# Optimization experiments

Measured on AMD Instinct MI355X. Metric: run time of the kernel, lower is better.

The kernel has to match this reference:

```python
import jax, jax.numpy as jnp
import numpy as np

B, NB, NV, H = 512, 3, 64, 256
CS = (40, 40)          # child branch lengths
COUP = (16, 48)        # parent vertices where child branches attach
IN = 9


def setup_inputs() -> dict:
    key = jax.random.key(0)
    ks = jax.random.split(key, 24)

    def w(k, shape, fan_in):
        return jax.random.uniform(k, shape, jnp.float32, -1.0, 1.0) / np.sqrt(fan_in)

    return {
        "current_vertices": jax.random.normal(ks[0], (B, NB, NV, 3), jnp.float32),
        "previous_vertices": jax.random.normal(ks[1], (B, NB, NV, 3), jnp.float32),
        "clamped_target_hints": jax.random.normal(ks[2], (B, NB, NV, 3), jnp.float32),
        # encoder
        "enc_w1": w(ks[3], (IN, H), IN), "enc_b1": w(ks[4], (H,), IN),
        "enc_w2": w(ks[5], (H, H), H), "enc_b2": w(ks[6], (H,), H),
        # child-sum tree-LSTM cell (bottom-up)
        "W_iou": w(ks[7], (H, 3 * H), H), "b_iou": w(ks[8], (3 * H,), H),
        "U_iou": w(ks[9], (H, 3 * H), H),
        "W_f": w(ks[10], (H, H), H), "b_f": w(ks[11], (H,), H),
        "U_f": w(ks[12], (H, H), H),
        # torch.nn.LSTMCell (top-down), gate order i,f,g,o
        "W_ih": w(ks[13], (H, 4 * H), H), "b_ih": w(ks[14], (4 * H,), H),
        "W_hh": w(ks[15], (H, 4 * H), H), "b_hh": w(ks[16], (4 * H,), H),
        # decoder
        "dec_w1": w(ks[17], (2 * H, H), 2 * H), "dec_b1": w(ks[18], (H,), 2 * H),
        "dec_w2": w(ks[19], (H, 3), H), "dec_b2": w(ks[20], (3,), H),
    }


def _forward(cv, pv, hints,
             enc_w1, enc_b1, enc_w2, enc_b2,
             W_iou, b_iou, U_iou, W_f, b_f, U_f,
             W_ih, b_ih, W_hh, b_hh,
             dec_w1, dec_b1, dec_w2, dec_b2):
    Bsz = cv.shape[0]
    nv = cv.shape[2]
    dt = cv.dtype
    feats = jnp.concatenate([cv, cv - pv, hints], axis=-1)            # [B,NB,NV,9]
    enc = jnp.maximum(feats @ enc_w1 + enc_b1, 0.0) @ enc_w2 + enc_b2  # [B,NB,NV,H]
    zero = jnp.zeros((Bsz, H), dt)

    # --- bottom-up: child-sum cell. A leaf with a single all-zero child is
    # mathematically identical to a zero initial carry (U_* have no bias),
    # so each chain is a plain scan from leaf toward vertex 0.
    def bu_chain_step(carry, x):
        h_prev, c_prev = carry
        iou = x @ W_iou + b_iou + h_prev @ U_iou
        i, o, u = jnp.split(iou, 3, axis=-1)
        f = jax.nn.sigmoid(x @ W_f + b_f + h_prev @ U_f)
        c = jax.nn.sigmoid(i) * jnp.tanh(u) + f * c_prev
        h = jax.nn.sigmoid(o) * jnp.tanh(c)
        return (h, c), (h, c)

    # child branches: leaf (v=L-1) -> v=0
    roots_h, roots_c, child_bu = [], [], []
    for k, L in enumerate(CS):
        xs = jnp.transpose(enc[:, k + 1, :L], (1, 0, 2))[::-1]  # time-major, reversed
        _, (hs, cs) = jax.lax.scan(bu_chain_step, (zero, zero), xs)
        hs, cs = hs[::-1], cs[::-1]                              # [L,B,H] indexed by v
        roots_h.append(hs[0]); roots_c.append(cs[0])
        child_bu.append((hs, cs))

    # coupled-child states injected at coupling vertices of the parent chain
    K = len(CS)
    coup_h = jnp.zeros((nv, K, Bsz, H), dt)
    coup_c = jnp.zeros_like(coup_h)
    coup_m = jnp.zeros((nv, K), dt)
    for k, ci in enumerate(COUP):
        coup_h = coup_h.at[ci, k].set(roots_h[k])
        coup_c = coup_c.at[ci, k].set(roots_c[k])
        coup_m = coup_m.at[ci, k].set(1.0)

    def bu_parent_step(carry, inp):
        h_prev, c_prev = carry
        x, ch, cc, m = inp  # ch,cc: [K,B,H]; m: [K]
        h_sum = h_prev + (m[:, None, None] * ch).sum(0)
        iou = x @ W_iou + b_iou + h_sum @ U_iou
        i, o, u = jnp.split(iou, 3, axis=-1)
        wf = x @ W_f + b_f
        fc = jax.nn.sigmoid(wf + h_prev @ U_f) * c_prev
        fc = fc + (m[:, None, None] * jax.nn.sigmoid(wf[None] + ch @ U_f) * cc).sum(0)
        c = jax.nn.sigmoid(i) * jnp.tanh(u) + fc
        h = jax.nn.sigmoid(o) * jnp.tanh(c)
        return (h, c), (h, c)

    xs0 = jnp.transpose(enc[:, 0], (1, 0, 2))  # [NV,B,H]
    _, (p_hs, p_cs) = jax.lax.scan(
        bu_parent_step, (zero, zero),
        (xs0[::-1], coup_h[::-1], coup_c[::-1], coup_m[::-1]))
    p_hs, p_cs = p_hs[::-1], p_cs[::-1]

    bu_h = jnp.zeros((Bsz, NB, nv, H), dt)
    bu_c = jnp.zeros_like(bu_h)
    bu_h = bu_h.at[:, 0].set(jnp.transpose(p_hs, (1, 0, 2)))
    bu_c = bu_c.at[:, 0].set(jnp.transpose(p_cs, (1, 0, 2)))
    for k, L in enumerate(CS):
        hs, cs = child_bu[k]
        bu_h = bu_h.at[:, k + 1, :L].set(jnp.transpose(hs, (1, 0, 2)))
        bu_c = bu_c.at[:, k + 1, :L].set(jnp.transpose(cs, (1, 0, 2)))

    # --- top-down: standard LSTMCell chains
    def td_step(carry, x):
        h, c = carry
        g = x @ W_ih + b_ih + h @ W_hh + b_hh
        i, f, gg, o = jnp.split(g, 4, axis=-1)
        c = jax.nn.sigmoid(f) * c + jax.nn.sigmoid(i) * jnp.tanh(gg)
        h = jax.nn.sigmoid(o) * jnp.tanh(c)
        return (h, c), (h, c)

    _, (t_hs, t_cs) = jax.lax.scan(td_step, (bu_h[:, 0, 0], bu_c[:, 0, 0]), xs0[1:])
    td_p_h = jnp.concatenate([bu_h[:, 0, 0][None], t_hs], 0)  # [NV,B,H]
    td_p_c = jnp.concatenate([bu_c[:, 0, 0][None], t_cs], 0)

    td_h = jnp.zeros_like(bu_h)
    td_h = td_h.at[:, 0].set(jnp.transpose(td_p_h, (1, 0, 2)))
    for k, L in enumerate(CS):
        xs = jnp.transpose(enc[:, k + 1, :L], (1, 0, 2))
        _, (hs, _) = jax.lax.scan(td_step, (td_p_h[COUP[k]], td_p_c[COUP[k]]), xs)
        td_h = td_h.at[:, k + 1, :L].set(jnp.transpose(hs, (1, 0, 2)))

    comb = jnp.concatenate([bu_h, td_h], axis=-1)  # [B,NB,NV,2H]
    delta = jnp.maximum(comb @ dec_w1 + dec_b1, 0.0) @ dec_w2 + dec_b2
    pred = cv + delta
    mask = jnp.ones((NB, nv, 1), dt)
    for k, L in enumerate(CS):
        mask = mask.at[k + 1, L:].set(0.0)
    return pred * mask[None]


def reference(current_vertices, previous_vertices, clamped_target_hints,
              enc_w1, enc_b1, enc_w2, enc_b2,
              W_iou, b_iou, U_iou, W_f, b_f, U_f,
              W_ih, b_ih, W_hh, b_hh,
              dec_w1, dec_b1, dec_w2, dec_b2):
    return _forward(current_vertices, previous_vertices, clamped_target_hints,
                    enc_w1, enc_b1, enc_w2, enc_b2,
                    W_iou, b_iou, U_iou, W_f, b_f, U_f,
                    W_ih, b_ih, W_hh, b_hh,
                    dec_w1, dec_b1, dec_w2, dec_b2)
```

## Files before the change

kernel.cpp:

```cpp
#include <hip/hip_runtime.h>
#include <hip/hip_bf16.h>
#include <hip/hip_fp8.h>


constexpr int Hd    = 256;
constexpr int NBv   = 3;
constexpr int NVv   = 64;
constexpr int BATCH = 512;
constexpr long long NROWS = (long long)BATCH * NBv * NVv;
constexpr int CLEN = 40;
constexpr int CI0 = 16, CI1 = 48;

typedef __hip_bfloat16 bf16;
typedef unsigned short ushort;
typedef unsigned char u8;
typedef __attribute__((ext_vector_type(8))) short short8;
typedef __attribute__((ext_vector_type(4))) float f32x4;
typedef __attribute__((ext_vector_type(2))) long longx2;

__device__ __forceinline__ float sigf(float x)   { return 1.f / (1.f + __expf(-x)); }
__device__ __forceinline__ float tanh_f(float x) { return 1.f - 2.f / (__expf(2.f * x) + 1.f); }

__device__ __forceinline__ ushort f2bf(float x) {
  unsigned u = __float_as_uint(x);
  return (ushort)((u + 0x7FFFu + ((u >> 16) & 1u)) >> 16);
}
__device__ __forceinline__ float bf2f(ushort u) {
  return __uint_as_float(((unsigned)u) << 16);
}
__device__ __forceinline__ u8 f2fp8(float x) {
  __hip_fp8_e4m3 q(x);
  return (u8)q.__x;
}

#define STEPSYNC() { \
    asm volatile("s_waitcnt lgkmcnt(0)" ::: "memory"); \
    __builtin_amdgcn_s_barrier(); }

__global__ __launch_bounds__(256) void pack_bu8_kernel(
    const float* __restrict__ W_iou, const float* __restrict__ W_f,
    const float* __restrict__ U_iou, const float* __restrict__ U_f,
    u8* __restrict__ out)
{
  int u = blockIdx.x * 256 + threadIdx.x;
  int s = u & 1, l = (u >> 1) & 63, T = u >> 7;
  int kp = T & 7, nt = T >> 3;
  int ks = kp * 2 + s;
  int k0 = ks * 32 + (l >> 4) * 8;
  int n  = nt * 16 + (l & 15);
  unsigned long long r = 0;
#pragma unroll
  for (int j = 0; j < 8; ++j) {
    int k = k0 + j;
    float v;
    if (k < 256) v = (n < 768) ? W_iou[k * 768 + n] : W_f[k * 256 + (n - 768)];
    else         v = (n < 768) ? U_iou[(k - 256) * 768 + n] : U_f[(k - 256) * 256 + (n - 768)];
    r |= ((unsigned long long)f2fp8(v)) << (8 * j);
  }
  *(unsigned long long*)(out + (size_t)u * 8) = r;
}

__global__ __launch_bounds__(256) void pack_td8_kernel(
    const float* __restrict__ W_ih, const float* __restrict__ W_hh,
    u8* __restrict__ out)
{
  int u = blockIdx.x * 256 + threadIdx.x;
  int s = u & 1, l = (u >> 1) & 63, T = u >> 7;
  int kp = T & 7, nt = T >> 3;
  int ks = kp * 2 + s;
  int k0 = ks * 32 + (l >> 4) * 8;
  int n  = nt * 16 + (l & 15);
  unsigned long long r = 0;
#pragma unroll
  for (int j = 0; j < 8; ++j) {
    int k = k0 + j;
    float v = (k < 256) ? W_ih[k * 1024 + n] : W_hh[(k - 256) * 1024 + n];
    r |= ((unsigned long long)f2fp8(v)) << (8 * j);
  }
  *(unsigned long long*)(out + (size_t)u * 8) = r;
}

__global__ __launch_bounds__(256) void pack_wfx8_kernel(
    const float* __restrict__ W_f, u8* __restrict__ out)
{
  int u = blockIdx.x * 256 + threadIdx.x;
  int s = u & 1, l = (u >> 1) & 63, T = u >> 7;
  int kp = T & 3, nt = T >> 2;
  int ks = kp * 2 + s;
  int k0 = ks * 32 + (l >> 4) * 8;
  int n  = nt * 16 + (l & 15);
  unsigned long long r = 0;
#pragma unroll
  for (int j = 0; j < 8; ++j)
    r |= ((unsigned long long)f2fp8(W_f[(k0 + j) * 256 + n])) << (8 * j);
  *(unsigned long long*)(out + (size_t)u * 8) = r;
}

__global__ __launch_bounds__(256) void pack_encw2_kernel(
    const float* __restrict__ w2, ushort* __restrict__ out)
{
  int idx = blockIdx.x * 256 + threadIdx.x;
  int j = idx & 7, l = (idx >> 3) & 63, T = idx >> 9;
  int ks = T & 7, nt = T >> 3;
  int k = ks * 32 + (l >> 4) * 8 + j;
  int n = nt * 16 + (l & 15);
  out[idx] = f2bf(w2[k * 256 + n]);
}

__global__ __launch_bounds__(256) void pack_decw1_kernel(
    const float* __restrict__ w1, ushort* __restrict__ out)
{
  int idx = blockIdx.x * 256 + threadIdx.x;
  int j = idx & 7, l = (idx >> 3) & 63, T = idx >> 9;
  int ks = T & 15, nt = T >> 4;
  int k = ks * 32 + (l >> 4) * 8 + j;
  int n = nt * 16 + (l & 15);
  out[idx] = f2bf(w1[k * 256 + n]);
}

__global__ __launch_bounds__(256) void pack_decw2_kernel(
    const float* __restrict__ w2, ushort* __restrict__ out)
{
  int idx = blockIdx.x * 256 + threadIdx.x;
  int j = idx & 7, l = (idx >> 3) & 63, T = idx >> 9;
  int ks = T & 7;
  int k = ks * 32 + (l >> 4) * 8 + j;
  int n = l & 15;
  out[idx] = (n < 3) ? f2bf(w2[k * 3 + n]) : (ushort)0;
}

__device__ __forceinline__ short8 ldA16(const ushort* buf, int row, int kbyte) {
  int off = (row * 512 + kbyte) ^ ((row & 7) << 4);
  return *(const short8*)((const char*)buf + off);
}
__device__ __forceinline__ short8 ldA1024(const ushort* buf, int row, int kbyte) {
  int off = (row * 1024 + kbyte) ^ ((row & 7) << 4);
  return *(const short8*)((const char*)buf + off);
}
#define STA(BUF, R, JJ, BITS) { \
    int off_ = ((R) * 512 + (JJ) * 2) ^ (((R) & 7) << 4); \
    (BUF)[off_ >> 1] = (BITS); }
#define STA8(BUF, R, JJ, B8) { \
    int off_ = ((R) * 256 + (JJ)) ^ (((R) & 7) << 3); \
    (BUF)[off_] = (B8); }

__global__ __launch_bounds__(256) void enc_kernel(
    const float* __restrict__ cv, const float* __restrict__ pv,
    const float* __restrict__ hints,
    const float* __restrict__ w1, const float* __restrict__ b1,
    const ushort* __restrict__ w2p, const float* __restrict__ b2,
    ushort* __restrict__ enc)
{
  __shared__ float fs[32][10];
  __shared__ ushort h1L[32 * 256];
  const long long row0 = (long long)blockIdx.x * 32;
  const int tid = threadIdx.x;
  if (tid < 96) {
    int r = tid / 3, c = tid % 3;
    long long row = row0 + r;
    float a = cv[row * 3 + c];
    fs[r][c]     = a;
    fs[r][3 + c] = a - pv[row * 3 + c];
    fs[r][6 + c] = hints[row * 3 + c];
  }
  __syncthreads();
  {
    const int j = tid;
    float wc[9];
#pragma unroll
    for (int i = 0; i < 9; ++i) wc[i] = w1[i * 256 + j];
    const float bb = b1[j];
    for (int r = 0; r < 32; ++r) {
      float a = bb;
#pragma unroll
      for (int i = 0; i < 9; ++i) a += fs[r][i] * wc[i];
      ushort hb = f2bf(fmaxf(a, 0.f));
      STA(h1L, r, j, hb);
    }
  }
  __syncthreads();
  const int lane = tid & 63, w = tid >> 6;
  const int col = lane & 15, krow = lane >> 4, kb = krow * 16;
  const f32x4 zf4 = {0.f, 0.f, 0.f, 0.f};
  f32x4 acc[2][4];
#pragma unroll
  for (int m = 0; m < 2; ++m)
#pragma unroll
    for (int g = 0; g < 4; ++g) acc[m][g] = zf4;
#pragma unroll
  for (int ks = 0; ks < 8; ++ks) {
    short8 A[2];
#pragma unroll
    for (int m = 0; m < 2; ++m) A[m] = ldA16(h1L, m * 16 + col, ks * 64 + kb);
#pragma unroll
    for (int g = 0; g < 4; ++g) {
      short8 b = *(const short8*)(w2p + ((((w * 4 + g) * 8 + ks) * 64 + lane)) * 8);
#pragma unroll
      for (int m = 0; m < 2; ++m)
        acc[m][g] = __builtin_amdgcn_mfma_f32_16x16x32_bf16(A[m], b, acc[m][g], 0, 0, 0);
    }
  }
#pragma unroll
  for (int g = 0; g < 4; ++g) {
    const int jj = (w * 4 + g) * 16 + col;
    const float bb = b2[jj];
#pragma unroll
    for (int m = 0; m < 2; ++m)
#pragma unroll
      for (int q = 0; q < 4; ++q) {
        long long row = row0 + m * 16 + krow * 4 + q;
        enc[row * 256 + jj] = f2bf(acc[m][g][q] + bb);
      }
  }
}

template<int MT>
__device__ __forceinline__ void gemm_main8(
    const u8* __restrict__ W, const u8* __restrict__ AxL,
    const u8* __restrict__ AhL, f32x4 (&acc)[MT][4], int w, int lane)
{
  const int col = lane & 15;
  const int kb  = (lane >> 4) * 8;
  const int sw  = (col & 7) << 3;
#pragma unroll 4
  for (int kp = 0; kp < 8; ++kp) {
    const u8* Ab = (kp < 4) ? AxL : AhL;
    const int ksl = (kp & 3) * 2;
    long a[MT][2];
#pragma unroll
    for (int m = 0; m < MT; ++m) {
      int base = (m * 16 + col) * 256 + ksl * 32 + kb;
      a[m][0] = *(const long*)(Ab + ((base) ^ sw));
      a[m][1] = *(const long*)(Ab + ((base + 32) ^ sw));
    }
#pragma unroll
    for (int g = 0; g < 4; ++g) {
      longx2 bq = *(const longx2*)(W + ((size_t)(((g * 16 + w) * 8 + kp) * 64 + lane) << 4));
#pragma unroll
      for (int m = 0; m < MT; ++m) {
        acc[m][g] = __builtin_amdgcn_mfma_f32_16x16x32_fp8_fp8(a[m][0], bq[0], acc[m][g], 0, 0, 0);
        acc[m][g] = __builtin_amdgcn_mfma_f32_16x16x32_fp8_fp8(a[m][1], bq[1], acc[m][g], 0, 0, 0);
      }
    }
  }
}

__device__ __forceinline__ void gemm_side8(
    const u8* __restrict__ Wbu, const u8* __restrict__ Wfx,
    const u8* __restrict__ Rhb, const u8* __restrict__ AxL,
    f32x4 (&accs)[4], f32x4& accw, int w, int lane)
{
  const int col = lane & 15;
  const int kb  = (lane >> 4) * 8;
  const int sw  = (col & 7) << 3;
#pragma unroll
  for (int kp = 0; kp < 4; ++kp) {
    const int base = col * 256 + kp * 64 + kb;
    long ar0 = *(const long*)(Rhb + ((base) ^ sw));
    long ar1 = *(const long*)(Rhb + ((base + 32) ^ sw));
#pragma unroll
    for (int g = 0; g < 4; ++g) {
      longx2 bq = *(const longx2*)(Wbu + ((size_t)(((g * 16 + w) * 8 + kp + 4) * 64 + lane) << 4));
      accs[g] = __builtin_amdgcn_mfma_f32_16x16x32_fp8_fp8(ar0, bq[0], accs[g], 0, 0, 0);
      accs[g] = __builtin_amdgcn_mfma_f32_16x16x32_fp8_fp8(ar1, bq[1], accs[g], 0, 0, 0);
    }
    long ax0 = *(const long*)(AxL + ((base) ^ sw));
    long ax1 = *(const long*)(AxL + ((base + 32) ^ sw));
    longx2 bw = *(const longx2*)(Wfx + ((size_t)((w * 4 + kp) * 64 + lane) << 4));
    accw = __builtin_amdgcn_mfma_f32_16x16x32_fp8_fp8(ax0, bw[0], accw, 0, 0, 0);
    accw = __builtin_amdgcn_mfma_f32_16x16x32_fp8_fp8(ax1, bw[1], accw, 0, 0, 0);
  }
}

#define ZACC(MT_, A_) { \
  _Pragma("unroll") for (int m_ = 0; m_ < MT_; ++m_) \
  _Pragma("unroll") for (int g_ = 0; g_ < 4; ++g_) A_[m_][g_] = zf4; }

__global__ __launch_bounds__(1024, 4) void seq_kernel(
    const ushort* enc,
    const u8* __restrict__ Wbu, const u8* __restrict__ Wtd,
    const u8* __restrict__ Wfx,
    const float* __restrict__ b_iou, const float* __restrict__ b_f,
    const float* __restrict__ b_ih,  const float* __restrict__ b_hh,
    ushort* __restrict__ bu_h, ushort* td_h)
{
  __shared__ u8 Axb[2][32 * 256];
  __shared__ u8 Ahb[2][32 * 256];
  __shared__ u8 Rh[2][16 * 256];

  const int tid  = threadIdx.x;
  const int lane = tid & 63;
  const int w    = tid >> 6;
  const int b0   = blockIdx.x * 16;
  const int col  = lane & 15;
  const int krow = lane >> 4;
  const f32x4 zf4 = {0.f, 0.f, 0.f, 0.f};

  const int jj = w * 16 + col;
  const float bi0 = b_iou[jj], bi1 = b_iou[256 + jj], bi2 = b_iou[512 + jj];
  const float bfv = b_f[jj];
  const float bt0 = b_ih[jj]       + b_hh[jj];
  const float bt1 = b_ih[256 + jj] + b_hh[256 + jj];
  const float bt2 = b_ih[512 + jj] + b_hh[512 + jj];
  const float bt3 = b_ih[768 + jj] + b_hh[768 + jj];

  float c2[2][4];
  float rc0[4], rc1[4];
  float sc0[4], sc1[4];

#define SLOAD32(V, XV) { \
    int rr_ = tid >> 5, ch_ = tid & 31; \
    int mt_ = rr_ >> 4, br_ = rr_ & 15; \
    long long rowg_ = ((long long)(b0 + br_) * NBv + (mt_ + 1)) * NVv + (V); \
    XV = *(const short8*)(enc + rowg_ * 256 + ch_ * 8); }

#define SLOAD16(V, XV) if (tid < 512) { \
    int rr_ = tid >> 5, ch_ = tid & 31; \
    long long rowg_ = ((long long)(b0 + rr_) * NBv) * NVv + (V); \
    XV = *(const short8*)(enc + rowg_ * 256 + ch_ * 8); }

#define SWRITE(DST, XV, GUARD) if (GUARD) { \
    int rr_ = tid >> 5, ch_ = tid & 31; \
    unsigned long long r_ = 0; \
    _Pragma("unroll") for (int e_ = 0; e_ < 8; ++e_) \
      r_ |= ((unsigned long long)f2fp8(bf2f((ushort)XV[e_]))) << (8 * e_); \
    *(unsigned long long*)((DST) + (((rr_ * 256 + ch_ * 8) ^ ((rr_ & 7) << 3)))) = r_; }

  {
    *(unsigned long long*)(&Ahb[0][tid * 8]) = 0ull;
    short8 xv; SLOAD32(CLEN - 1, xv);
#pragma unroll
    for (int m = 0; m < 2; ++m)
#pragma unroll
      for (int q = 0; q < 4; ++q) c2[m][q] = 0.f;
    SWRITE(Axb[0], xv, true);
    __syncthreads();
    for (int s = 0; s < CLEN; ++s) {
      const int v = CLEN - 1 - s, pp = s & 1;
      short8 xn;
      if (s < CLEN - 1) SLOAD32(v - 1, xn);
      f32x4 acc[2][4]; ZACC(2, acc);
      gemm_main8<2>(Wbu, Axb[pp], Ahb[pp], acc, w, lane);
#pragma unroll
      for (int m = 0; m < 2; ++m)
#pragma unroll
        for (int q = 0; q < 4; ++q) {
          const int br = krow * 4 + q;
          float I = acc[m][0][q] + bi0;
          float O = acc[m][1][q] + bi1;
          float U = acc[m][2][q] + bi2;
          float F = acc[m][3][q] + bfv;
          float cn = sigf(I) * tanh_f(U) + sigf(F) * c2[m][q];
          float hn = sigf(O) * tanh_f(cn);
          c2[m][q] = cn;
          u8 hq = f2fp8(hn);
          STA8(Ahb[pp ^ 1], m * 16 + br, jj, hq);
          long long rowg = ((long long)(b0 + br) * NBv + (m + 1)) * NVv + v;
          bu_h[rowg * 256 + jj] = f2bf(hn);
          if (v == 0) {
            STA8(Rh[m], br, jj, hq);
            if (m == 0) rc0[q] = cn; else rc1[q] = cn;
          }
        }
      if (s < CLEN - 1) SWRITE(Axb[pp ^ 1], xn, true);
      STEPSYNC();
    }
  }

  {
    if (tid < 512) *(unsigned long long*)(&Ahb[0][tid * 8]) = 0ull;
    short8 xv = {};
    SLOAD16(NVv - 1, xv);
#pragma unroll
    for (int q = 0; q < 4; ++q) c2[0][q] = 0.f;
    SWRITE(Axb[0], xv, (tid < 512));
    __syncthreads();
    for (int s = 0; s < NVv; ++s) {
      const int v = NVv - 1 - s, pp = s & 1;
      short8 xn = {};
      if (s < NVv - 1) SLOAD16(v - 1, xn);
      f32x4 acc[1][4]; ZACC(1, acc);
      gemm_main8<1>(Wbu, Axb[pp], Ahb[pp], acc, w, lane);
      const int ck = (v == CI0) ? 0 : ((v == CI1) ? 1 : -1);
      f32x4 accs[4]; f32x4 accw;
      if (ck >= 0) {
#pragma unroll
        for (int g = 0; g < 4; ++g) accs[g] = zf4;
        accw = zf4;
        const u8* Rp = (ck == 0) ? Rh[0] : Rh[1];
        gemm_side8(Wbu, Wfx, Rp, Axb[pp], accs, accw, w, lane);
      }
#pragma unroll
      for (int q = 0; q < 4; ++q) {
        const int br = krow * 4 + q;
        float I  = acc[0][0][q] + bi0;
        float O  = acc[0][1][q] + bi1;
        float U  = acc[0][2][q] + bi2;
        float F1 = acc[0][3][q] + bfv;
        float fc = sigf(F1) * c2[0][q];
        if (ck >= 0) {
          I += accs[0][q]; O += accs[1][q]; U += accs[2][q];
          float wfx = accw[q] + bfv;
          float rcv = (ck == 0) ? rc0[q] : rc1[q];
          fc += sigf(wfx + accs[3][q]) * rcv;
        }
        float cn = sigf(I) * tanh_f(U) + fc;
        float hn = sigf(O) * tanh_f(cn);
        c2[0][q] = cn;
        u8 hq = f2fp8(hn);
        STA8(Ahb[pp ^ 1], br, jj, hq);
        long long rowg = ((long long)(b0 + br) * NBv) * NVv + v;
        bu_h[rowg * 256 + jj] = f2bf(hn);
        if (v == 0) td_h[rowg * 256 + jj] = f2bf(hn);
      }
      if (s < NVv - 1) SWRITE(Axb[pp ^ 1], xn, (tid < 512));
      STEPSYNC();
    }
  }

  {
    short8 xv = {};
    SLOAD16(1, xv);
    SWRITE(Axb[0], xv, (tid < 512));
    __syncthreads();
    for (int s = 0; s < NVv - 1; ++s) {
      const int v = 1 + s, pp = s & 1;
      short8 xn = {};
      if (s < NVv - 2) SLOAD16(v + 1, xn);
      f32x4 acc[1][4]; ZACC(1, acc);
      gemm_main8<1>(Wtd, Axb[pp], Ahb[pp], acc, w, lane);
#pragma unroll
      for (int q = 0; q < 4; ++q) {
        const int br = krow * 4 + q;
        float I = acc[0][0][q] + bt0;
        float F = acc[0][1][q] + bt1;
        float G = acc[0][2][q] + bt2;
        float O = acc[0][3][q] + bt3;
        float cn = sigf(F) * c2[0][q] + sigf(I) * tanh_f(G);
        float hn = sigf(O) * tanh_f(cn);
        c2[0][q] = cn;
        u8 hq = f2fp8(hn);
        STA8(Ahb[pp ^ 1], br, jj, hq);
        long long rowg = ((long long)(b0 + br) * NBv) * NVv + v;
        td_h[rowg * 256 + jj] = f2bf(hn);
        if (v == CI0) { STA8(Rh[0], br, jj, hq); sc0[q] = cn; }
        if (v == CI1) { STA8(Rh[1], br, jj, hq); sc1[q] = cn; }
      }
      if (s < NVv - 2) SWRITE(Axb[pp ^ 1], xn, (tid < 512));
      STEPSYNC();
    }
  }

  {
    {
      int rr = tid >> 5, ch = tid & 31;
      int mt = rr >> 4, br = rr & 15;
      unsigned long long vv = *(const unsigned long long*)(
          &Rh[mt][0] + (((br * 256 + ch * 8) ^ ((br & 7) << 3))));
      *(unsigned long long*)(&Ahb[0][0] + (((rr * 256 + ch * 8) ^ ((rr & 7) << 3)))) = vv;
    }
    short8 xv; SLOAD32(0, xv);
#pragma unroll
    for (int m = 0; m < 2; ++m)
#pragma unroll
      for (int q = 0; q < 4; ++q)
        c2[m][q] = (m == 0) ? sc0[q] : sc1[q];
    SWRITE(Axb[0], xv, true);
    __syncthreads();
    for (int s = 0; s < CLEN; ++s) {
      const int v = s, pp = s & 1;
      short8 xn;
      if (s < CLEN - 1) SLOAD32(v + 1, xn);
      f32x4 acc[2][4]; ZACC(2, acc);
      gemm_main8<2>(Wtd, Axb[pp], Ahb[pp], acc, w, lane);
#pragma unroll
      for (int m = 0; m < 2; ++m)
#pragma unroll
        for (int q = 0; q < 4; ++q) {
          const int br = krow * 4 + q;
          float I = acc[m][0][q] + bt0;
          float F = acc[m][1][q] + bt1;
          float G = acc[m][2][q] + bt2;
          float O = acc[m][3][q] + bt3;
          float cn = sigf(F) * c2[m][q] + sigf(I) * tanh_f(G);
          float hn = sigf(O) * tanh_f(cn);
          c2[m][q] = cn;
          u8 hq = f2fp8(hn);
          STA8(Ahb[pp ^ 1], m * 16 + br, jj, hq);
          long long rowg = ((long long)(b0 + br) * NBv + (m + 1)) * NVv + v;
          td_h[rowg * 256 + jj] = f2bf(hn);
        }
      if (s < CLEN - 1) SWRITE(Axb[pp ^ 1], xn, true);
      STEPSYNC();
    }
  }
}

__global__ __launch_bounds__(256) void dec_kernel(
    const ushort* __restrict__ bu_h, const ushort* __restrict__ td_h,
    const float* __restrict__ cv,
    const ushort* __restrict__ w1p, const float* __restrict__ b1,
    const ushort* __restrict__ w2p, const float* __restrict__ b2,
    float* __restrict__ out)
{
  __shared__ ushort combL[32 * 512];
  __shared__ ushort hidL[32 * 256];
  const long long row0 = (long long)blockIdx.x * 32;
  const int tid = threadIdx.x;

#pragma unroll
  for (int h = 0; h < 8; ++h) {
    int cid = tid + h * 256;
    int rr = cid >> 6, ch = cid & 63;
    long long row = row0 + rr;
    short8 v = (ch < 32)
        ? *(const short8*)(bu_h + row * 256 + ch * 8)
        : *(const short8*)(td_h + row * 256 + (ch - 32) * 8);
    *(short8*)((char*)combL + ((rr * 1024 + ch * 16) ^ ((rr & 7) << 4))) = v;
  }
  __syncthreads();

  const int lane = tid & 63, w = tid >> 6;
  const int col = lane & 15, krow = lane >> 4, kb = krow * 16;
  const f32x4 zf4 = {0.f, 0.f, 0.f, 0.f};
  f32x4 acc[2][4];
#pragma unroll
  for (int m = 0; m < 2; ++m)
#pragma unroll
    for (int g = 0; g < 4; ++g) acc[m][g] = zf4;
#pragma unroll 4
  for (int ks = 0; ks < 16; ++ks) {
    short8 A[2];
#pragma unroll
    for (int m = 0; m < 2; ++m) A[m] = ldA1024(combL, m * 16 + col, ks * 64 + kb);
#pragma unroll
    for (int g = 0; g < 4; ++g) {
      short8 b = *(const short8*)(w1p + ((((w * 4 + g) * 16 + ks) * 64 + lane)) * 8);
#pragma unroll
      for (int m = 0; m < 2; ++m)
        acc[m][g] = __builtin_amdgcn_mfma_f32_16x16x32_bf16(A[m], b, acc[m][g], 0, 0, 0);
    }
  }
#pragma unroll
  for (int g = 0; g < 4; ++g) {
    const int jj = (w * 4 + g) * 16 + col;
    const float bb = b1[jj];
#pragma unroll
    for (int m = 0; m < 2; ++m)
#pragma unroll
      for (int q = 0; q < 4; ++q) {
        ushort hb = f2bf(fmaxf(acc[m][g][q] + bb, 0.f));
        STA(hidL, m * 16 + krow * 4 + q, jj, hb);
      }
  }
  __syncthreads();

  if (w == 0) {
    f32x4 acc2[2]; acc2[0] = zf4; acc2[1] = zf4;
#pragma unroll
    for (int ks = 0; ks < 8; ++ks) {
      short8 bv = *(const short8*)(w2p + ((ks * 64 + lane)) * 8);
#pragma unroll
      for (int m = 0; m < 2; ++m) {
        short8 A = ldA16(hidL, m * 16 + col, ks * 64 + kb);
        acc2[m] = __builtin_amdgcn_mfma_f32_16x16x32_bf16(A, bv, acc2[m], 0, 0, 0);
      }
    }
    if (col < 3) {
      const float bb = b2[col];
#pragma unroll
      for (int m = 0; m < 2; ++m)
#pragma unroll
        for (int q = 0; q < 4; ++q) {
          long long row = row0 + m * 16 + krow * 4 + q;
          int v  = (int)(row & 63);
          int br = (int)((row >> 6) % 3);
          float res = 0.f;
          if (br == 0 || v < CLEN)
            res = cv[row * 3 + col] + acc2[m][q] + bb;
          out[row * 3 + col] = res;
        }
    }
  }
}

extern "C" void kernel_launch(void* const* d_in, const int* in_sizes, int n_in,
                              void* d_out, int out_size, void* d_ws, size_t ws_size,
                              hipStream_t stream) {
  const float* cv     = (const float*)d_in[0];
  const float* pv     = (const float*)d_in[1];
  const float* hints  = (const float*)d_in[2];
  const float* enc_w1 = (const float*)d_in[3];
  const float* enc_b1 = (const float*)d_in[4];
  const float* enc_w2 = (const float*)d_in[5];
  const float* enc_b2 = (const float*)d_in[6];
  const float* W_iou  = (const float*)d_in[7];
  const float* b_iou  = (const float*)d_in[8];
  const float* U_iou  = (const float*)d_in[9];
  const float* W_f    = (const float*)d_in[10];
  const float* b_f    = (const float*)d_in[11];
  const float* U_f    = (const float*)d_in[12];
  const float* W_ih   = (const float*)d_in[13];
  const float* b_ih   = (const float*)d_in[14];
  const float* W_hh   = (const float*)d_in[15];
  const float* b_hh   = (const float*)d_in[16];
  const float* dec_w1 = (const float*)d_in[17];
  const float* dec_b1 = (const float*)d_in[18];
  const float* dec_w2 = (const float*)d_in[19];
  const float* dec_b2 = (const float*)d_in[20];

  size_t act = (size_t)NROWS * 256;
  size_t need = 2 * act * 2
              + 2 * (size_t)524288 + 65536
              + (65536 + 131072 + 4096) * 2;
  if (ws_size < need) return;

  ushort* encW   = (ushort*)d_ws;
  ushort* buh    = encW + act;
  u8*     Wbu8   = (u8*)(buh + act);
  u8*     Wtd8   = Wbu8 + 524288;
  u8*     Wfx8   = Wtd8 + 524288;
  ushort* encw2p = (ushort*)(Wfx8 + 65536);
  ushort* decw1p = encw2p + 65536;
  ushort* decw2p = decw1p + 131072;

  pack_bu8_kernel<<<256, 256, 0, stream>>>(W_iou, W_f, U_iou, U_f, Wbu8);
  pack_td8_kernel<<<256, 256, 0, stream>>>(W_ih, W_hh, Wtd8);
  pack_wfx8_kernel<<<32, 256, 0, stream>>>(W_f, Wfx8);
  pack_encw2_kernel<<<256, 256, 0, stream>>>(enc_w2, encw2p);
  pack_decw1_kernel<<<512, 256, 0, stream>>>(dec_w1, decw1p);
  pack_decw2_kernel<<<16, 256, 0, stream>>>(dec_w2, decw2p);

  enc_kernel<<<(int)(NROWS / 32), 256, 0, stream>>>(cv, pv, hints, enc_w1, enc_b1,
                                                    encw2p, enc_b2, encW);
  seq_kernel<<<BATCH / 16, 1024, 0, stream>>>(encW, Wbu8, Wtd8, Wfx8, b_iou, b_f,
                                              b_ih, b_hh, buh, encW);
  dec_kernel<<<(int)(NROWS / 32), 256, 0, stream>>>(buh, encW, cv, decw1p, dec_b1,
                                                    decw2p, dec_b2, (float*)d_out);
}
```

Before: 1.943 ms.

## Halve seq_kernel waves, give each two column tiles, keep gate-0 weights in registers

The recurrent kernel now launches 512 threads (8 waves) instead of 1024. Each wave computes two 16-column output tiles per gate, so every A fragment read from shared memory feeds twice as many MFMAs. The first gate's weight fragments for all eight k-slices are preloaded into registers (Bp) once per phase, instead of being refetched from global memory every timestep. The cost is higher register pressure and half as many waves to hide latency, so the kernel is pinned to 2 waves per EU, which may cause spills or less overlap in this latency-bound serial loop.

Measured after the change: 2.730 ms. +40.5%, slower.

```diff
diff --git a/kernel.cpp b/kernel.cpp
--- a/kernel.cpp
+++ b/kernel.cpp
@@ -217,7 +217,8 @@
 template<int MT>
 __device__ __forceinline__ void gemm_main8(
     const u8* __restrict__ W, const u8* __restrict__ AxL,
-    const u8* __restrict__ AhL, f32x4 (&acc)[MT][4], int w, int lane)
+    const u8* __restrict__ AhL, f32x4 (&acc)[MT][4][2],
+    const longx2 (&Bp)[2][8], int w, int lane)
 {
   const int col = lane & 15;
   const int kb  = (lane >> 4) * 8;
@@ -234,21 +235,30 @@
       a[m][1] = *(const long*)(Ab + ((base + 32) ^ sw));
     }
 #pragma unroll
-    for (int g = 0; g < 4; ++g) {
-      longx2 bq = *(const longx2*)(W + ((size_t)(((g * 16 + w) * 8 + kp) * 64 + lane) << 4));
+    for (int p = 0; p < 2; ++p)
 #pragma unroll
       for (int m = 0; m < MT; ++m) {
-        acc[m][g] = __builtin_amdgcn_mfma_f32_16x16x32_fp8_fp8(a[m][0], bq[0], acc[m][g], 0, 0, 0);
-        acc[m][g] = __builtin_amdgcn_mfma_f32_16x16x32_fp8_fp8(a[m][1], bq[1], acc[m][g], 0, 0, 0);
-      }
-    }
+        acc[m][0][p] = __builtin_amdgcn_mfma_f32_16x16x32_fp8_fp8(a[m][0], Bp[p][kp][0], acc[m][0][p], 0, 0, 0);
+        acc[m][0][p] = __builtin_amdgcn_mfma_f32_16x16x32_fp8_fp8(a[m][1], Bp[p][kp][1], acc[m][0][p], 0, 0, 0);
+      }
+#pragma unroll
+    for (int g = 1; g < 4; ++g)
+#pragma unroll
+      for (int p = 0; p < 2; ++p) {
+        longx2 bq = *(const longx2*)(W + ((size_t)(((g * 16 + 2 * w + p) * 8 + kp) * 64 + lane) << 4));
+#pragma unroll
+        for (int m = 0; m < MT; ++m) {
+          acc[m][g][p] = __builtin_amdgcn_mfma_f32_16x16x32_fp8_fp8(a[m][0], bq[0], acc[m][g][p], 0, 0, 0);
+          acc[m][g][p] = __builtin_amdgcn_mfma_f32_16x16x32_fp8_fp8(a[m][1], bq[1], acc[m][g][p], 0, 0, 0);
+        }
+      }
   }
 }
 
 __device__ __forceinline__ void gemm_side8(
     const u8* __restrict__ Wbu, const u8* __restrict__ Wfx,
     const u8* __restrict__ Rhb, const u8* __restrict__ AxL,
-    f32x4 (&accs)[4], f32x4& accw, int w, int lane)
+    f32x4 (&accs)[4][2], f32x4 (&accw)[2], int w, int lane)
 {
   const int col = lane & 15;
   const int kb  = (lane >> 4) * 8;
@@ -259,24 +269,32 @@
     long ar0 = *(const long*)(Rhb + ((base) ^ sw));
     long ar1 = *(const long*)(Rhb + ((base + 32) ^ sw));
 #pragma unroll
-    for (int g = 0; g < 4; ++g) {
-      longx2 bq = *(const longx2*)(Wbu + ((size_t)(((g * 16 + w) * 8 + kp + 4) * 64 + lane) << 4));
-      accs[g] = __builtin_amdgcn_mfma_f32_16x16x32_fp8_fp8(ar0, bq[0], accs[g], 0, 0, 0);
-      accs[g] = __builtin_amdgcn_mfma_f32_16x16x32_fp8_fp8(ar1, bq[1], accs[g], 0, 0, 0);
-    }
+    for (int g = 0; g < 4; ++g)
+#pragma unroll
+      for (int p = 0; p < 2; ++p) {
+        longx2 bq = *(const longx2*)(Wbu + ((size_t)(((g * 16 + 2 * w + p) * 8 + kp + 4) * 64 + lane) << 4));
+        accs[g][p] = __builtin_amdgcn_mfma_f32_16x16x32_fp8_fp8(ar0, bq[0], accs[g][p], 0, 0, 0);
+        accs[g][p] = __builtin_amdgcn_mfma_f32_16x16x32_fp8_fp8(ar1, bq[1], accs[g][p], 0, 0, 0);
+      }
     long ax0 = *(const long*)(AxL + ((base) ^ sw));
     long ax1 = *(const long*)(AxL + ((base + 32) ^ sw));
-    longx2 bw = *(const longx2*)(Wfx + ((size_t)((w * 4 + kp) * 64 + lane) << 4));
-    accw = __builtin_amdgcn_mfma_f32_16x16x32_fp8_fp8(ax0, bw[0], accw, 0, 0, 0);
-    accw = __builtin_amdgcn_mfma_f32_16x16x32_fp8_fp8(ax1, bw[1], accw, 0, 0, 0);
+#pragma unroll
+    for (int p = 0; p < 2; ++p) {
+      longx2 bw = *(const longx2*)(Wfx + ((size_t)(((2 * w + p) * 4 + kp) * 64 + lane) << 4));
+      accw[p] = __builtin_amdgcn_mfma_f32_16x16x32_fp8_fp8(ax0, bw[0], accw[p], 0, 0, 0);
+      accw[p] = __builtin_amdgcn_mfma_f32_16x16x32_fp8_fp8(ax1, bw[1], accw[p], 0, 0, 0);
+    }
   }
 }
 
 #define ZACC(MT_, A_) { \
   _Pragma("unroll") for (int m_ = 0; m_ < MT_; ++m_) \
-  _Pragma("unroll") for (int g_ = 0; g_ < 4; ++g_) A_[m_][g_] = zf4; }
-
-__global__ __launch_bounds__(1024, 4) void seq_kernel(
+  _Pragma("unroll") for (int g_ = 0; g_ < 4; ++g_) \
+  _Pragma("unroll") for (int p_ = 0; p_ < 2; ++p_) A_[m_][g_][p_] = zf4; }
+
+__global__ __launch_bounds__(512, 2)
+__attribute__((amdgpu_waves_per_eu(2, 2)))
+void seq_kernel(
     const ushort* enc,
     const u8* __restrict__ Wbu, const u8* __restrict__ Wtd,
     const u8* __restrict__ Wfx,
@@ -296,30 +314,49 @@
   const int krow = lane >> 4;
   const f32x4 zf4 = {0.f, 0.f, 0.f, 0.f};
 
-  const int jj = w * 16 + col;
-  const float bi0 = b_iou[jj], bi1 = b_iou[256 + jj], bi2 = b_iou[512 + jj];
-  const float bfv = b_f[jj];
-  const float bt0 = b_ih[jj]       + b_hh[jj];
-  const float bt1 = b_ih[256 + jj] + b_hh[256 + jj];
-  const float bt2 = b_ih[512 + jj] + b_hh[512 + jj];
-  const float bt3 = b_ih[768 + jj] + b_hh[768 + jj];
-
-  float c2[2][4];
-  float rc0[4], rc1[4];
-  float sc0[4], sc1[4];
-
-#define SLOAD32(V, XV) { \
-    int rr_ = tid >> 5, ch_ = tid & 31; \
-    int mt_ = rr_ >> 4, br_ = rr_ & 15; \
-    long long rowg_ = ((long long)(b0 + br_) * NBv + (mt_ + 1)) * NVv + (V); \
-    XV = *(const short8*)(enc + rowg_ * 256 + ch_ * 8); }
-
-#define SLOAD16(V, XV) if (tid < 512) { \
+  float bi0[2], bi1[2], bi2[2], bfv[2], bt0[2], bt1[2], bt2[2], bt3[2];
+#pragma unroll
+  for (int p = 0; p < 2; ++p) {
+    int jj = (2 * w + p) * 16 + col;
+    bi0[p] = b_iou[jj]; bi1[p] = b_iou[256 + jj]; bi2[p] = b_iou[512 + jj];
+    bfv[p] = b_f[jj];
+    bt0[p] = b_ih[jj]       + b_hh[jj];
+    bt1[p] = b_ih[256 + jj] + b_hh[256 + jj];
+    bt2[p] = b_ih[512 + jj] + b_hh[512 + jj];
+    bt3[p] = b_ih[768 + jj] + b_hh[768 + jj];
+  }
+
+  float c2[2][2][4];
+  float rc0[2][4], rc1[2][4];
+  float sc0[2][4], sc1[2][4];
+
+  longx2 Bp[2][8];
+#define LOADBP(W_) { \
+    _Pragma("unroll") for (int kp_ = 0; kp_ < 8; ++kp_) \
+    _Pragma("unroll") for (int p_ = 0; p_ < 2; ++p_) \
+      Bp[p_][kp_] = *(const longx2*)((W_) + ((size_t)(((2 * w + p_) * 8 + kp_) * 64 + lane) << 4)); }
+
+#define SLOAD32(V, XV2) { \
+    _Pragma("unroll") for (int h_ = 0; h_ < 2; ++h_) { \
+      int cid_ = tid + h_ * 512; int rr_ = cid_ >> 5, ch_ = cid_ & 31; \
+      int mt_ = rr_ >> 4, br_ = rr_ & 15; \
+      long long rowg_ = ((long long)(b0 + br_) * NBv + (mt_ + 1)) * NVv + (V); \
+      XV2[h_] = *(const short8*)(enc + rowg_ * 256 + ch_ * 8); } }
+
+#define SWRITE32(DST, XV2) { \
+    _Pragma("unroll") for (int h_ = 0; h_ < 2; ++h_) { \
+      int cid_ = tid + h_ * 512; int rr_ = cid_ >> 5, ch_ = cid_ & 31; \
+      unsigned long long r_ = 0; \
+      _Pragma("unroll") for (int e_ = 0; e_ < 8; ++e_) \
+        r_ |= ((unsigned long long)f2fp8(bf2f((ushort)XV2[h_][e_]))) << (8 * e_); \
+      *(unsigned long long*)((DST) + (((rr_ * 256 + ch_ * 8) ^ ((rr_ & 7) << 3)))) = r_; } }
+
+#define SLOAD16(V, XV) { \
     int rr_ = tid >> 5, ch_ = tid & 31; \
     long long rowg_ = ((long long)(b0 + rr_) * NBv) * NVv + (V); \
     XV = *(const short8*)(enc + rowg_ * 256 + ch_ * 8); }
 
-#define SWRITE(DST, XV, GUARD) if (GUARD) { \
+#define SWRITE16(DST, XV) { \
     int rr_ = tid >> 5, ch_ = tid & 31; \
     unsigned long long r_ = 0; \
     _Pragma("unroll") for (int e_ = 0; e_ < 8; ++e_) \
@@ -327,170 +364,198 @@
     *(unsigned long long*)((DST) + (((rr_ * 256 + ch_ * 8) ^ ((rr_ & 7) << 3)))) = r_; }
 
   {
-    *(unsigned long long*)(&Ahb[0][tid * 8]) = 0ull;
-    short8 xv; SLOAD32(CLEN - 1, xv);
+    LOADBP(Wbu);
+#pragma unroll
+    for (int h_ = 0; h_ < 2; ++h_)
+      *(unsigned long long*)(&Ahb[0][(tid + h_ * 512) * 8]) = 0ull;
+    short8 xv2[2]; SLOAD32(CLEN - 1, xv2);
 #pragma unroll
     for (int m = 0; m < 2; ++m)
 #pragma unroll
-      for (int q = 0; q < 4; ++q) c2[m][q] = 0.f;
-    SWRITE(Axb[0], xv, true);
+      for (int p = 0; p < 2; ++p)
+#pragma unroll
+        for (int q = 0; q < 4; ++q) c2[m][p][q] = 0.f;
+    SWRITE32(Axb[0], xv2);
     __syncthreads();
     for (int s = 0; s < CLEN; ++s) {
       const int v = CLEN - 1 - s, pp = s & 1;
-      short8 xn;
-      if (s < CLEN - 1) SLOAD32(v - 1, xn);
-      f32x4 acc[2][4]; ZACC(2, acc);
-      gemm_main8<2>(Wbu, Axb[pp], Ahb[pp], acc, w, lane);
+      short8 xn2[2];
+      if (s < CLEN - 1) SLOAD32(v - 1, xn2);
+      f32x4 acc[2][4][2]; ZACC(2, acc);
+      gemm_main8<2>(Wbu, Axb[pp], Ahb[pp], acc, Bp, w, lane);
 #pragma unroll
       for (int m = 0; m < 2; ++m)
 #pragma unroll
-        for (int q = 0; q < 4; ++q) {
-          const int br = krow * 4 + q;
-          float I = acc[m][0][q] + bi0;
-          float O = acc[m][1][q] + bi1;
-          float U = acc[m][2][q] + bi2;
-          float F = acc[m][3][q] + bfv;
-          float cn = sigf(I) * tanh_f(U) + sigf(F) * c2[m][q];
-          float hn = sigf(O) * tanh_f(cn);
-          c2[m][q] = cn;
-          u8 hq = f2fp8(hn);
-          STA8(Ahb[pp ^ 1], m * 16 + br, jj, hq);
-          long long rowg = ((long long)(b0 + br) * NBv + (m + 1)) * NVv + v;
-          bu_h[rowg * 256 + jj] = f2bf(hn);
-          if (v == 0) {
-            STA8(Rh[m], br, jj, hq);
-            if (m == 0) rc0[q] = cn; else rc1[q] = cn;
+        for (int p = 0; p < 2; ++p) {
+          const int jj = (2 * w + p) * 16 + col;
+#pragma unroll
+          for (int q = 0; q < 4; ++q) {
+            const int br = krow * 4 + q;
+            float I = acc[m][0][p][q] + bi0[p];
+            float O = acc[m][1][p][q] + bi1[p];
+            float U = acc[m][2][p][q] + bi2[p];
+            float F = acc[m][3][p][q] + bfv[p];
+            float cn = sigf(I) * tanh_f(U) + sigf(F) * c2[m][p][q];
+            float hn = sigf(O) * tanh_f(cn);
+            c2[m][p][q] = cn;
+            u8 hq = f2fp8(hn);
+            STA8(Ahb[pp ^ 1], m * 16 + br, jj, hq);
+            long long rowg = ((long long)(b0 + br) * NBv + (m + 1)) * NVv + v;
+            bu_h[rowg * 256 + jj] = f2bf(hn);
+            if (v == 0) {
+              STA8(Rh[m], br, jj, hq);
+              if (m == 0) rc0[p][q] = cn; else rc1[p][q] = cn;
+            }
           }
         }
-      if (s < CLEN - 1) SWRITE(Axb[pp ^ 1], xn, true);
+      if (s < CLEN - 1) SWRITE32(Axb[pp ^ 1], xn2);
       STEPSYNC();
     }
   }
 
   {
-    if (tid < 512) *(unsigned long long*)(&Ahb[0][tid * 8]) = 0ull;
-    short8 xv = {};
-    SLOAD16(NVv - 1, xv);
-#pragma unroll
-    for (int q = 0; q < 4; ++q) c2[0][q] = 0.f;
-    SWRITE(Axb[0], xv, (tid < 512));
+    *(unsigned long long*)(&Ahb[0][tid * 8]) = 0ull;
+    short8 xv; SLOAD16(NVv - 1, xv);
+#pragma unroll
+    for (int p = 0; p < 2; ++p)
+#pragma unroll
+      for (int q = 0; q < 4; ++q) c2[0][p][q] = 0.f;
+    SWRITE16(Axb[0], xv);
     __syncthreads();
     for (int s = 0; s < NVv; ++s) {
       const int v = NVv - 1 - s, pp = s & 1;
       short8 xn = {};
       if (s < NVv - 1) SLOAD16(v - 1, xn);
-      f32x4 acc[1][4]; ZACC(1, acc);
-      gemm_main8<1>(Wbu, Axb[pp], Ahb[pp], acc, w, lane);
+      f32x4 acc[1][4][2]; ZACC(1, acc);
+      gemm_main8<1>(Wbu, Axb[pp], Ahb[pp], acc, Bp, w, lane);
       const int ck = (v == CI0) ? 0 : ((v == CI1) ? 1 : -1);
-      f32x4 accs[4]; f32x4 accw;
+      f32x4 accs[4][2]; f32x4 accw[2];
       if (ck >= 0) {
 #pragma unroll
-        for (int g = 0; g < 4; ++g) accs[g] = zf4;
-        accw = zf4;
+        for (int g = 0; g < 4; ++g)
+#pragma unroll
+          for (int p = 0; p < 2; ++p) accs[g][p] = zf4;
+        accw[0] = zf4; accw[1] = zf4;
         const u8* Rp = (ck == 0) ? Rh[0] : Rh[1];
         gemm_side8(Wbu, Wfx, Rp, Axb[pp], accs, accw, w, lane);
       }
 #pragma unroll
-      for (int q = 0; q < 4; ++q) {
-        const int br = krow * 4 + q;
-        float I  = acc[0][0][q] + bi0;
-        float O  = acc[0][1][q] + bi1;
-        float U  = acc[0][2][q] + bi2;
-        float F1 = acc[0][3][q] + bfv;
-        float fc = sigf(F1) * c2[0][q];
-        if (ck >= 0) {
-          I += accs[0][q]; O += accs[1][q]; U += accs[2][q];
-          float wfx = accw[q] + bfv;
-          float rcv = (ck == 0) ? rc0[q] : rc1[q];
-          fc += sigf(wfx + accs[3][q]) * rcv;
+      for (int p = 0; p < 2; ++p) {
+        const int jj = (2 * w + p) * 16 + col;
+#pragma unroll
+        for (int q = 0; q < 4; ++q) {
+          const int br = krow * 4 + q;
+          float I  = acc[0][0][p][q] + bi0[p];
+          float O  = acc[0][1][p][q] + bi1[p];
+          float U  = acc[0][2][p][q] + bi2[p];
+          float F1 = acc[0][3][p][q] + bfv[p];
+          float fc = sigf(F1) * c2[0][p][q];
+          if (ck >= 0) {
+            I += accs[0][p][q]; O += accs[1][p][q]; U += accs[2][p][q];
+            float wfx = accw[p][q] + bfv[p];
+            float rcv = (ck == 0) ? rc0[p][q] : rc1[p][q];
+            fc += sigf(wfx + accs[3][p][q]) * rcv;
+          }
+          float cn = sigf(I) * tanh_f(U) + fc;
+          float hn = sigf(O) * tanh_f(cn);
+          c2[0][p][q] = cn;
+          u8 hq = f2fp8(hn);
+          STA8(Ahb[pp ^ 1], br, jj, hq);
+          long long rowg = ((long long)(b0 + br) * NBv) * NVv + v;
+          bu_h[rowg * 256 + jj] = f2bf(hn);
+          if (v == 0) td_h[rowg * 256 + jj] = f2bf(hn);
         }
-        float cn = sigf(I) * tanh_f(U) + fc;
-        float hn = sigf(O) * tanh_f(cn);
-        c2[0][q] = cn;
-        u8 hq = f2fp8(hn);
-        STA8(Ahb[pp ^ 1], br, jj, hq);
-        long long rowg = ((long long)(b0 + br) * NBv) * NVv + v;
-        bu_h[rowg * 256 + jj] = f2bf(hn);
-        if (v == 0) td_h[rowg * 256 + jj] = f2bf(hn);
-      }
-      if (s < NVv - 1) SWRITE(Axb[pp ^ 1], xn, (tid < 512));
+      }
+      if (s < NVv - 1) SWRITE16(Axb[pp ^ 1], xn);
       STEPSYNC();
     }
   }
 
   {
-    short8 xv = {};
-    SLOAD16(1, xv);
-    SWRITE(Axb[0], xv, (tid < 512));
+    LOADBP(Wtd);
+    short8 xv; SLOAD16(1, xv);
+    SWRITE16(Axb[0], xv);
     __syncthreads();
     for (int s = 0; s < NVv - 1; ++s) {
       const int v = 1 + s, pp = s & 1;
       short8 xn = {};
       if (s < NVv - 2) SLOAD16(v + 1, xn);
-      f32x4 acc[1][4]; ZACC(1, acc);
-      gemm_main8<1>(Wtd, Axb[pp], Ahb[pp], acc, w, lane);
-#pragma unroll
-      for (int q = 0; q < 4; ++q) {
-        const int br = krow * 4 + q;
-        float I = acc[0][0][q] + bt0;
-        float F = acc[0][1][q] + bt1;
-        float G = acc[0][2][q] + bt2;
-        float O = acc[0][3][q] + bt3;
-        float cn = sigf(F) * c2[0][q] + sigf(I) * tanh_f(G);
-        float hn = sigf(O) * tanh_f(cn);
-        c2[0][q] = cn;
-        u8 hq = f2fp8(hn);
-        STA8(Ahb[pp ^ 1], br, jj, hq);
-        long long rowg = ((long long)(b0 + br) * NBv) * NVv + v;
-        td_h[rowg * 256 + jj] = f2bf(hn);
-        if (v == CI0) { STA8(Rh[0], br, jj, hq); sc0[q] = cn; }
-        if (v == CI1) { STA8(Rh[1], br, jj, hq); sc1[q] = cn; }
-      }
-      if (s < NVv - 2) SWRITE(Axb[pp ^ 1], xn, (tid < 512));
+      f32x4 acc[1][4][2]; ZACC(1, acc);
+      gemm_main8<1>(Wtd, Axb[pp], Ahb[pp], acc, Bp, w, lane);
+#pragma unroll
+      for (int p = 0; p < 2; ++p) {
+        const int jj = (2 * w + p) * 16 + col;
+#pragma unroll
+        for (int q = 0; q < 4; ++q) {
+          const int br = krow * 4 + q;
+          float I = acc[0][0][p][q] + bt0[p];
+          float F = acc[0][1][p][q] + bt1[p];
+          float G = acc[0][2][p][q] + bt2[p];
+          float O = acc[0][3][p][q] + bt3[p];
+          float cn = sigf(F) * c2[0][p][q] + sigf(I) * tanh_f(G);
+          float hn = sigf(O) * tanh_f(cn);
+          c2[0][p][q] = cn;
+          u8 hq = f2fp8(hn);
+          STA8(Ahb[pp ^ 1], br, jj, hq);
+          long long rowg = ((long long)(b0 + br) * NBv) * NVv + v;
+          td_h[rowg * 256 + jj] = f2bf(hn);
+          if (v == CI0) { STA8(Rh[0], br, jj, hq); sc0[p][q] = cn; }
+          if (v == CI1) { STA8(Rh[1], br, jj, hq); sc1[p][q] = cn; }
+        }
+      }
+      if (s < NVv - 2) SWRITE16(Axb[pp ^ 1], xn);
       STEPSYNC();
     }
   }
 
   {
-    {
-      int rr = tid >> 5, ch = tid & 31;
+#pragma unroll
+    for (int h_ = 0; h_ < 2; ++h_) {
+      int cid = tid + h_ * 512;
+      int rr = cid >> 5, ch = cid & 31;
       int mt = rr >> 4, br = rr & 15;
       unsigned long long vv = *(const unsigned long long*)(
           &Rh[mt][0] + (((br * 256 + ch * 8) ^ ((br & 7) << 3))));
       *(unsigned long long*)(&Ahb[0][0] + (((rr * 256 + ch * 8) ^ ((rr & 7) << 3)))) = vv;
     }
-    short8 xv; SLOAD32(0, xv);
+    short8 xv2[2]; SLOAD32(0, xv2);
 #pragma unroll
     for (int m = 0; m < 2; ++m)
 #pragma unroll
-      for (int q = 0; q < 4; ++q)
-        c2[m][q] = (m == 0) ? sc0[q] : sc1[q];
-    SWRITE(Axb[0], xv, true);
+      for (int p = 0; p < 2; ++p)
+#pragma unroll
+        for (int q = 0; q < 4; ++q)
+          c2[m][p][q] = (m == 0) ? sc0[p][q] : sc1[p][q];
+    SWRITE32(Axb[0], xv2);
     __syncthreads();
     for (int s = 0; s < CLEN; ++s) {
       const int v = s, pp = s & 1;
-      short8 xn;
-      if (s < CLEN - 1) SLOAD32(v + 1, xn);
-      f32x4 acc[2][4]; ZACC(2, acc);
-      gemm_main8<2>(Wtd, Axb[pp], Ahb[pp], acc, w, lane);
+      short8 xn2[2];
+      if (s < CLEN - 1) SLOAD32(v + 1, xn2);
+      f32x4 acc[2][4][2]; ZACC(2, acc);
+      gemm_main8<2>(Wtd, Axb[pp], Ahb[pp], acc, Bp, w, lane);
 #pragma unroll
       for (int m = 0; m < 2; ++m)
 #pragma unroll
-        for (int q = 0; q < 4; ++q) {
-          const int br = krow * 4 + q;
-          float I = acc[m][0][q] + bt0;
-          float F = acc[m][1][q] + bt1;
-          float G = acc[m][2][q] + bt2;
-          float O = acc[m][3][q] + bt3;
-          float cn = sigf(F) * c2[m][q] + sigf(I) * tanh_f(G);
-          float hn = sigf(O) * tanh_f(cn);
-          c2[m][q] = cn;
-          u8 hq = f2fp8(hn);
-          STA8(Ahb[pp ^ 1], m * 16 + br, jj, hq);
-          long long rowg = ((long long)(b0 + br) * NBv + (m + 1)) * NVv + v;
-          td_h[rowg * 256 + jj] = f2bf(hn);
+        for (int p = 0; p < 2; ++p) {
+          const int jj = (2 * w + p) * 16 + col;
+#pragma unroll
+          for (int q = 0; q < 4; ++q) {
+            const int br = krow * 4 + q;
+            float I = acc[m][0][p][q] + bt0[p];
+            float F = acc[m][1][p][q] + bt1[p];
+            float G = acc[m][2][p][q] + bt2[p];
+            float O = acc[m][3][p][q] + bt3[p];
+            float cn = sigf(F) * c2[m][p][q] + sigf(I) * tanh_f(G);
+            float hn = sigf(O) * tanh_f(cn);
+            c2[m][p][q] = cn;
+            u8 hq = f2fp8(hn);
+            STA8(Ahb[pp ^ 1], m * 16 + br, jj, hq);
+            long long rowg = ((long long)(b0 + br) * NBv + (m + 1)) * NVv + v;
+            td_h[rowg * 256 + jj] = f2bf(hn);
+          }
         }
-      if (s < CLEN - 1) SWRITE(Axb[pp ^ 1], xn, true);
+      if (s < CLEN - 1) SWRITE32(Axb[pp ^ 1], xn2);
       STEPSYNC();
     }
   }
@@ -633,8 +698,8 @@
 
   enc_kernel<<<(int)(NROWS / 32), 256, 0, stream>>>(cv, pv, hints, enc_w1, enc_b1,
                                                     encw2p, enc_b2, encW);
-  seq_kernel<<<BATCH / 16, 1024, 0, stream>>>(encW, Wbu8, Wtd8, Wfx8, b_iou, b_f,
-                                              b_ih, b_hh, buh, encW);
+  seq_kernel<<<BATCH / 16, 512, 0, stream>>>(encW, Wbu8, Wtd8, Wfx8, b_iou, b_f,
+                                             b_ih, b_hh, buh, encW);
   dec_kernel<<<(int)(NROWS / 32), 256, 0, stream>>>(buh, encW, cv, decw1p, dec_b1,
                                                     decw2p, dec_b2, (float*)d_out);
 }
```
